# Kernel tuning notes

Hardware: AMD Instinct MI355X
Metric: run time of the kernel (lower is better)

## Reference

```python
import jax, jax.numpy as jnp
import numpy as np

IN_F = 4096
OUT_F = 4096
SPARSITY = 0.9
NNZ = round((1.0 - SPARSITY) * IN_F * OUT_F)  # 1677722
BATCH = 4096


def setup_inputs() -> dict:
    key = jax.random.key(0)
    k1, k2, k3, k4 = jax.random.split(key, 4)
    x = jax.random.normal(k1, (BATCH, IN_F), dtype=jnp.float32)
    # Kaiming-ish scale for sparse fan-in
    weights = jax.random.normal(k2, (NNZ,), dtype=jnp.float32) * 0.02
    row = jax.random.randint(k3, (NNZ,), 0, OUT_F, dtype=jnp.int32)
    col = jax.random.randint(k4, (NNZ,), 0, IN_F, dtype=jnp.int32)
    indices = jnp.stack([row, col], axis=0)  # (2, nnz) like the torch buffer
    active_mask = jnp.ones((NNZ,), dtype=bool)
    return {
        "x": x,
        "weights": weights,
        "indices": indices,
        "active_mask": active_mask,
        "out_features": OUT_F,
        "in_features": IN_F,
    }


def reference(x, weights, indices, active_mask, out_features, in_features):
    # Torch forward: select active edges, build COO (out,in), coalesce
    # (sums duplicate indices), then y = (W @ x^T)^T.
    # Equivalent math: zero inactive weights, scatter-add into dense W,
    # then a dense matmul. Duplicates are summed by .add, matching coalesce.
    w = jnp.where(active_mask, weights, jnp.zeros((), dtype=weights.dtype))
    W = jnp.zeros((out_features, in_features), dtype=x.dtype)
    W = W.at[indices[0], indices[1]].add(w)  # (out, in)
    return x @ W.T  # (B, out)
```

## Files before the change

### kernel.cpp

```cpp
#include <hip/hip_runtime.h>
#include <cstdint>
#include <cstddef>

#define IN_F  4096
#define OUT_F 4096
#define BATCH 4096

typedef __bf16 bf16_t;
typedef __bf16 bf16x8 __attribute__((ext_vector_type(8)));
typedef float  f32x4  __attribute__((ext_vector_type(4)));

__device__ __forceinline__ unsigned short f32_to_bf16_rne(float f) {
  union { float f; unsigned int u; } v;
  v.f = f;
  unsigned int u = v.u;
  return (unsigned short)((u + 0x7FFFu + ((u >> 16) & 1u)) >> 16);
}

__device__ __forceinline__ uint4 cvt8(float4 a, float4 b) {
  uint4 o;
  o.x = (unsigned)f32_to_bf16_rne(a.x) | ((unsigned)f32_to_bf16_rne(a.y) << 16);
  o.y = (unsigned)f32_to_bf16_rne(a.z) | ((unsigned)f32_to_bf16_rne(a.w) << 16);
  o.z = (unsigned)f32_to_bf16_rne(b.x) | ((unsigned)f32_to_bf16_rne(b.y) << 16);
  o.w = (unsigned)f32_to_bf16_rne(b.z) | ((unsigned)f32_to_bf16_rne(b.w) << 16);
  return o;
}

#define WU16 ((OUT_F * IN_F) / 8)
#define XUNITS ((BATCH * IN_F) / 8)

__global__ __launch_bounds__(256) void init_zero_cvtx(
    uint4* __restrict__ Wbfv, const float4* __restrict__ xin,
    uint4* __restrict__ xbf) {
  const uint4 z = {0u, 0u, 0u, 0u};
  for (int u = blockIdx.x * 256 + threadIdx.x; u < WU16 + XUNITS;
       u += gridDim.x * 256) {
    if (u < WU16) {
      Wbfv[u] = z;
    } else {
      const int i = u - WU16;
      xbf[i] = cvt8(xin[2 * i], xin[2 * i + 1]);
    }
  }
}

__global__ __launch_bounds__(256) void scatter_bf16(
    const float* __restrict__ w, const int* __restrict__ rows,
    const int* __restrict__ cols, const int* __restrict__ mask,
    unsigned* __restrict__ Wpk, int nnz) {
  int i = blockIdx.x * 256 + threadIdx.x;
  if (i >= nnz) return;
  if (mask[i] == 0) return;
  const unsigned h = f32_to_bf16_rne(w[i]);
  const size_t e = (size_t)rows[i] * IN_F + cols[i];
  const unsigned data = (e & 1) ? (h << 16) : h;
  unsigned* p = Wpk + (e >> 1);
  asm volatile("global_atomic_pk_add_bf16 %0, %1, off"
               :: "v"(p), "v"(data) : "memory");
}

#define A0_B 0
#define B0_B 32768
#define A1_B 65536
#define B1_B 98304
#define HALF 16384

#define STAGE(Xg, kpos, ldsbase) do {                                          \
  __builtin_amdgcn_global_load_lds(                                            \
    (const __attribute__((address_space(1))) void*)((Xg) + (size_t)srow * 4096 + (kpos) + schunk), \
    (__attribute__((address_space(3))) void*)(lds + (ldsbase) + tid * 16), 16, 0, 0); \
  __builtin_amdgcn_global_load_lds(                                            \
    (const __attribute__((address_space(1))) void*)((Xg) + (size_t)(srow + 128) * 4096 + (kpos) + schunk), \
    (__attribute__((address_space(3))) void*)(lds + (ldsbase) + 8192 + tid * 16), 16, 0, 0); \
} while (0)

#define LDALL(ab, bb) do {                                                     \
  a0 = *(const bf16x8*)(lds + (ab) + offA[0][0]);                              \
  a1 = *(const bf16x8*)(lds + (ab) + offA[0][1]);                              \
  a2 = *(const bf16x8*)(lds + (ab) + offA[0][2]);                              \
  a3 = *(const bf16x8*)(lds + (ab) + offA[0][3]);                              \
  a4 = *(const bf16x8*)(lds + (ab) + offA[1][0]);                              \
  a5 = *(const bf16x8*)(lds + (ab) + offA[1][1]);                              \
  a6 = *(const bf16x8*)(lds + (ab) + offA[1][2]);                              \
  a7 = *(const bf16x8*)(lds + (ab) + offA[1][3]);                              \
  b0 = *(const bf16x8*)(lds + (bb) + offB[0]);                                 \
  b1 = *(const bf16x8*)(lds + (bb) + offB[1]);                                 \
  b2 = *(const bf16x8*)(lds + (bb) + offB[2]);                                 \
  b3 = *(const bf16x8*)(lds + (bb) + offB[3]);                                 \
} while (0)

#define MQ(mh, A0_, A1_, A2_, A3_) do {                                        \
  acc[(mh)*4+0][0] = __builtin_amdgcn_mfma_f32_16x16x32_bf16(A0_, b0, acc[(mh)*4+0][0], 0, 0, 0); \
  acc[(mh)*4+0][1] = __builtin_amdgcn_mfma_f32_16x16x32_bf16(A0_, b1, acc[(mh)*4+0][1], 0, 0, 0); \
  acc[(mh)*4+0][2] = __builtin_amdgcn_mfma_f32_16x16x32_bf16(A0_, b2, acc[(mh)*4+0][2], 0, 0, 0); \
  acc[(mh)*4+0][3] = __builtin_amdgcn_mfma_f32_16x16x32_bf16(A0_, b3, acc[(mh)*4+0][3], 0, 0, 0); \
  acc[(mh)*4+1][0] = __builtin_amdgcn_mfma_f32_16x16x32_bf16(A1_, b0, acc[(mh)*4+1][0], 0, 0, 0); \
  acc[(mh)*4+1][1] = __builtin_amdgcn_mfma_f32_16x16x32_bf16(A1_, b1, acc[(mh)*4+1][1], 0, 0, 0); \
  acc[(mh)*4+1][2] = __builtin_amdgcn_mfma_f32_16x16x32_bf16(A1_, b2, acc[(mh)*4+1][2], 0, 0, 0); \
  acc[(mh)*4+1][3] = __builtin_amdgcn_mfma_f32_16x16x32_bf16(A1_, b3, acc[(mh)*4+1][3], 0, 0, 0); \
  acc[(mh)*4+2][0] = __builtin_amdgcn_mfma_f32_16x16x32_bf16(A2_, b0, acc[(mh)*4+2][0], 0, 0, 0); \
  acc[(mh)*4+2][1] = __builtin_amdgcn_mfma_f32_16x16x32_bf16(A2_, b1, acc[(mh)*4+2][1], 0, 0, 0); \
  acc[(mh)*4+2][2] = __builtin_amdgcn_mfma_f32_16x16x32_bf16(A2_, b2, acc[(mh)*4+2][2], 0, 0, 0); \
  acc[(mh)*4+2][3] = __builtin_amdgcn_mfma_f32_16x16x32_bf16(A2_, b3, acc[(mh)*4+2][3], 0, 0, 0); \
  acc[(mh)*4+3][0] = __builtin_amdgcn_mfma_f32_16x16x32_bf16(A3_, b0, acc[(mh)*4+3][0], 0, 0, 0); \
  acc[(mh)*4+3][1] = __builtin_amdgcn_mfma_f32_16x16x32_bf16(A3_, b1, acc[(mh)*4+3][1], 0, 0, 0); \
  acc[(mh)*4+3][2] = __builtin_amdgcn_mfma_f32_16x16x32_bf16(A3_, b2, acc[(mh)*4+3][2], 0, 0, 0); \
  acc[(mh)*4+3][3] = __builtin_amdgcn_mfma_f32_16x16x32_bf16(A3_, b3, acc[(mh)*4+3][3], 0, 0, 0); \
} while (0)

#define MFMA32() do { MQ(0, a0, a1, a2, a3); MQ(1, a4, a5, a6, a7); } while (0)

#define BAR()   __builtin_amdgcn_s_barrier()
#define LGKM0() do { asm volatile("s_waitcnt lgkmcnt(0)" ::: "memory");        \
                     __builtin_amdgcn_sched_barrier(0); } while (0)
#define VM(n)   asm volatile("s_waitcnt vmcnt(" #n ")" ::: "memory")
#define PRIO1() __builtin_amdgcn_s_setprio(1)
#define PRIO0() __builtin_amdgcn_s_setprio(0)

__global__ __launch_bounds__(512, 2) void gemm_bt_4ph(
    const bf16_t* __restrict__ A, const bf16_t* __restrict__ Bm,
    float* __restrict__ C) {
  __shared__ __align__(16) char lds[131072];

  const int tid  = threadIdx.x;
  const int lane = tid & 63;
  const int wave = tid >> 6;
  const int wm   = wave >> 2;
  const int wn   = wave & 3;

  const int sbid = (blockIdx.x & 7) * 32 + (blockIdx.x >> 3);
  const int bm   = sbid >> 4;
  const int bn   = sbid & 15;

  const int frow = lane & 15;
  const int c16  = (lane >> 4) * 16;

  int offA[2][4], offB[4];
#pragma unroll
  for (int mh = 0; mh < 2; ++mh)
#pragma unroll
    for (int mi = 0; mi < 4; ++mi) {
      int r = wm * 128 + mh * 64 + mi * 16 + frow;
      offA[mh][mi] = r * 64 + (c16 ^ (((r >> 1) & 3) << 4));
    }
#pragma unroll
  for (int ni = 0; ni < 4; ++ni) {
    int r = wn * 64 + ni * 16 + frow;
    offB[ni] = r * 64 + (c16 ^ (((r >> 1) & 3) << 4));
  }

  const int srow   = tid >> 2;
  const int schunk = ((tid & 3) ^ ((srow >> 1) & 3)) * 8;
  const bf16_t* Ag = A  + (size_t)bm * 256 * 4096;
  const bf16_t* Bg = Bm + (size_t)bn * 256 * 4096;

  f32x4 acc[8][4] = {};
  bf16x8 a0, a1, a2, a3, a4, a5, a6, a7, b0, b1, b2, b3;

  STAGE(Ag, 0,  A0_B);
  STAGE(Bg, 0,  B0_B);
  STAGE(Ag, 32, A0_B + HALF);
  STAGE(Bg, 32, B0_B + HALF);
  STAGE(Ag, 64, A1_B);
  STAGE(Bg, 64, B1_B);
  VM(8);
  BAR();

  int kb = 0;
#pragma unroll 1
  for (int i = 0; i < 31; ++i, kb += 128) {
    LDALL(A0_B, B0_B);
    STAGE(Ag, kb + 96, A1_B + HALF);
    STAGE(Bg, kb + 96, B1_B + HALF);
    BAR(); LGKM0(); PRIO1(); MFMA32(); PRIO0(); VM(8); BAR();
    LDALL(A0_B + HALF, B0_B + HALF);
    STAGE(Ag, kb + 128, A0_B);
    STAGE(Bg, kb + 128, B0_B);
    BAR(); LGKM0(); PRIO1(); MFMA32(); PRIO0(); VM(8); BAR();
    LDALL(A1_B, B1_B);
    STAGE(Ag, kb + 160, A0_B + HALF);
    STAGE(Bg, kb + 160, B0_B + HALF);
    BAR(); LGKM0(); PRIO1(); MFMA32(); PRIO0(); VM(8); BAR();
    LDALL(A1_B + HALF, B1_B + HALF);
    STAGE(Ag, kb + 192, A1_B);
    STAGE(Bg, kb + 192, B1_B);
    BAR(); LGKM0(); PRIO1(); MFMA32(); PRIO0(); VM(8); BAR();
  }

  LDALL(A0_B, B0_B);
  STAGE(Ag, 4064, A1_B + HALF);
  STAGE(Bg, 4064, B1_B + HALF);
  BAR(); LGKM0(); PRIO1(); MFMA32(); PRIO0(); VM(8); BAR();
  LDALL(A0_B + HALF, B0_B + HALF);
  BAR(); LGKM0(); PRIO1(); MFMA32(); PRIO0(); VM(4); BAR();
  LDALL(A1_B, B1_B);
  BAR(); LGKM0(); PRIO1(); MFMA32(); PRIO0(); VM(0); BAR();
  LDALL(A1_B + HALF, B1_B + HALF);
  LGKM0(); PRIO1(); MFMA32(); PRIO0();

#pragma unroll
  for (int mh = 0; mh < 2; ++mh)
#pragma unroll
    for (int mi = 0; mi < 4; ++mi)
#pragma unroll
      for (int ni = 0; ni < 4; ++ni) {
        const int row = bm * 256 + wm * 128 + mh * 64 + mi * 16 + (lane >> 4) * 4;
        const int col = bn * 256 + wn * 64 + ni * 16 + frow;
#pragma unroll
        for (int jj = 0; jj < 4; ++jj)
          C[(size_t)(row + jj) * 4096 + col] = acc[mh * 4 + mi][ni][jj];
      }
}

extern "C" void kernel_launch(void* const* d_in, const int* in_sizes, int n_in,
                              void* d_out, int out_size, void* d_ws, size_t ws_size,
                              hipStream_t stream) {
  const float* x     = (const float*)d_in[0];
  const float* wvals = (const float*)d_in[1];
  const int*   idx   = (const int*)d_in[2];
  const int*   mk    = (const int*)d_in[3];
  const int    nnz   = in_sizes[1];

  bf16_t* Wbf = (bf16_t*)d_ws;
  bf16_t* xbf = (bf16_t*)((char*)d_ws + (size_t)OUT_F * IN_F * sizeof(bf16_t));

  const size_t needed = (size_t)OUT_F * IN_F * 2 + (size_t)BATCH * IN_F * 2;
  if (ws_size < needed) return;

  init_zero_cvtx<<<2048, 256, 0, stream>>>(
      (uint4*)Wbf, (const float4*)x, (uint4*)xbf);

  scatter_bf16<<<(nnz + 255) / 256, 256, 0, stream>>>(
      wvals, idx, idx + nnz, mk, (unsigned*)Wbf, nnz);

  gemm_bt_4ph<<<256, 512, 0, stream>>>(xbf, Wbf, (float*)d_out);
}
```

Before: 212.3 us.

## Double-buffer LDS fragment registers to overlap LDS reads with MFMA

Splits the A/B fragment registers into two sets so that LDS reads for the next k-slice are issued while MFMAs consume the previous slice. Waits are relaxed to lgkmcnt(12) and vmcnt(4) so compute only waits for the older set. This removes the LDS-read latency exposed before each MFMA block, at the cost of 24 more VGPRs of fragments. With launch bounds of 2 waves per SIMD this may cause register pressure or spills, and it shifts the hazards between barriers and buffer reuse.

```diff
diff --git a/kernel.cpp b/kernel.cpp
--- a/kernel.cpp
+++ b/kernel.cpp
@@ -74,50 +74,53 @@
     (__attribute__((address_space(3))) void*)(lds + (ldsbase) + 8192 + tid * 16), 16, 0, 0); \
 } while (0)
 
-#define LDALL(ab, bb) do {                                                     \
-  a0 = *(const bf16x8*)(lds + (ab) + offA[0][0]);                              \
-  a1 = *(const bf16x8*)(lds + (ab) + offA[0][1]);                              \
-  a2 = *(const bf16x8*)(lds + (ab) + offA[0][2]);                              \
-  a3 = *(const bf16x8*)(lds + (ab) + offA[0][3]);                              \
-  a4 = *(const bf16x8*)(lds + (ab) + offA[1][0]);                              \
-  a5 = *(const bf16x8*)(lds + (ab) + offA[1][1]);                              \
-  a6 = *(const bf16x8*)(lds + (ab) + offA[1][2]);                              \
-  a7 = *(const bf16x8*)(lds + (ab) + offA[1][3]);                              \
-  b0 = *(const bf16x8*)(lds + (bb) + offB[0]);                                 \
-  b1 = *(const bf16x8*)(lds + (bb) + offB[1]);                                 \
-  b2 = *(const bf16x8*)(lds + (bb) + offB[2]);                                 \
-  b3 = *(const bf16x8*)(lds + (bb) + offB[3]);                                 \
-} while (0)
-
-#define MQ(mh, A0_, A1_, A2_, A3_) do {                                        \
-  acc[(mh)*4+0][0] = __builtin_amdgcn_mfma_f32_16x16x32_bf16(A0_, b0, acc[(mh)*4+0][0], 0, 0, 0); \
-  acc[(mh)*4+0][1] = __builtin_amdgcn_mfma_f32_16x16x32_bf16(A0_, b1, acc[(mh)*4+0][1], 0, 0, 0); \
-  acc[(mh)*4+0][2] = __builtin_amdgcn_mfma_f32_16x16x32_bf16(A0_, b2, acc[(mh)*4+0][2], 0, 0, 0); \
-  acc[(mh)*4+0][3] = __builtin_amdgcn_mfma_f32_16x16x32_bf16(A0_, b3, acc[(mh)*4+0][3], 0, 0, 0); \
-  acc[(mh)*4+1][0] = __builtin_amdgcn_mfma_f32_16x16x32_bf16(A1_, b0, acc[(mh)*4+1][0], 0, 0, 0); \
-  acc[(mh)*4+1][1] = __builtin_amdgcn_mfma_f32_16x16x32_bf16(A1_, b1, acc[(mh)*4+1][1], 0, 0, 0); \
-  acc[(mh)*4+1][2] = __builtin_amdgcn_mfma_f32_16x16x32_bf16(A1_, b2, acc[(mh)*4+1][2], 0, 0, 0); \
-  acc[(mh)*4+1][3] = __builtin_amdgcn_mfma_f32_16x16x32_bf16(A1_, b3, acc[(mh)*4+1][3], 0, 0, 0); \
-  acc[(mh)*4+2][0] = __builtin_amdgcn_mfma_f32_16x16x32_bf16(A2_, b0, acc[(mh)*4+2][0], 0, 0, 0); \
-  acc[(mh)*4+2][1] = __builtin_amdgcn_mfma_f32_16x16x32_bf16(A2_, b1, acc[(mh)*4+2][1], 0, 0, 0); \
-  acc[(mh)*4+2][2] = __builtin_amdgcn_mfma_f32_16x16x32_bf16(A2_, b2, acc[(mh)*4+2][2], 0, 0, 0); \
-  acc[(mh)*4+2][3] = __builtin_amdgcn_mfma_f32_16x16x32_bf16(A2_, b3, acc[(mh)*4+2][3], 0, 0, 0); \
-  acc[(mh)*4+3][0] = __builtin_amdgcn_mfma_f32_16x16x32_bf16(A3_, b0, acc[(mh)*4+3][0], 0, 0, 0); \
-  acc[(mh)*4+3][1] = __builtin_amdgcn_mfma_f32_16x16x32_bf16(A3_, b1, acc[(mh)*4+3][1], 0, 0, 0); \
-  acc[(mh)*4+3][2] = __builtin_amdgcn_mfma_f32_16x16x32_bf16(A3_, b2, acc[(mh)*4+3][2], 0, 0, 0); \
-  acc[(mh)*4+3][3] = __builtin_amdgcn_mfma_f32_16x16x32_bf16(A3_, b3, acc[(mh)*4+3][3], 0, 0, 0); \
-} while (0)
-
-#define MFMA32() do { MQ(0, a0, a1, a2, a3); MQ(1, a4, a5, a6, a7); } while (0)
-
-#define BAR()   __builtin_amdgcn_s_barrier()
-#define LGKM0() do { asm volatile("s_waitcnt lgkmcnt(0)" ::: "memory");        \
-                     __builtin_amdgcn_sched_barrier(0); } while (0)
-#define VM(n)   asm volatile("s_waitcnt vmcnt(" #n ")" ::: "memory")
-#define PRIO1() __builtin_amdgcn_s_setprio(1)
-#define PRIO0() __builtin_amdgcn_s_setprio(0)
-
-__global__ __launch_bounds__(512, 2) void gemm_bt_4ph(
+#define RDSET(ab, bb, S) do {                                                  \
+  a##S##0 = *(const bf16x8*)(lds + (ab) + offA[0][0]);                         \
+  a##S##1 = *(const bf16x8*)(lds + (ab) + offA[0][1]);                         \
+  a##S##2 = *(const bf16x8*)(lds + (ab) + offA[0][2]);                         \
+  a##S##3 = *(const bf16x8*)(lds + (ab) + offA[0][3]);                         \
+  a##S##4 = *(const bf16x8*)(lds + (ab) + offA[1][0]);                         \
+  a##S##5 = *(const bf16x8*)(lds + (ab) + offA[1][1]);                         \
+  a##S##6 = *(const bf16x8*)(lds + (ab) + offA[1][2]);                         \
+  a##S##7 = *(const bf16x8*)(lds + (ab) + offA[1][3]);                         \
+  b##S##0 = *(const bf16x8*)(lds + (bb) + offB[0]);                            \
+  b##S##1 = *(const bf16x8*)(lds + (bb) + offB[1]);                            \
+  b##S##2 = *(const bf16x8*)(lds + (bb) + offB[2]);                            \
+  b##S##3 = *(const bf16x8*)(lds + (bb) + offB[3]);                            \
+} while (0)
+
+#define MQ(mh, A0_,A1_,A2_,A3_, B0_,B1_,B2_,B3_) do {                          \
+  acc[(mh)*4+0][0] = __builtin_amdgcn_mfma_f32_16x16x32_bf16(A0_, B0_, acc[(mh)*4+0][0], 0, 0, 0); \
+  acc[(mh)*4+0][1] = __builtin_amdgcn_mfma_f32_16x16x32_bf16(A0_, B1_, acc[(mh)*4+0][1], 0, 0, 0); \
+  acc[(mh)*4+0][2] = __builtin_amdgcn_mfma_f32_16x16x32_bf16(A0_, B2_, acc[(mh)*4+0][2], 0, 0, 0); \
+  acc[(mh)*4+0][3] = __builtin_amdgcn_mfma_f32_16x16x32_bf16(A0_, B3_, acc[(mh)*4+0][3], 0, 0, 0); \
+  acc[(mh)*4+1][0] = __builtin_amdgcn_mfma_f32_16x16x32_bf16(A1_, B0_, acc[(mh)*4+1][0], 0, 0, 0); \
+  acc[(mh)*4+1][1] = __builtin_amdgcn_mfma_f32_16x16x32_bf16(A1_, B1_, acc[(mh)*4+1][1], 0, 0, 0); \
+  acc[(mh)*4+1][2] = __builtin_amdgcn_mfma_f32_16x16x32_bf16(A1_, B2_, acc[(mh)*4+1][2], 0, 0, 0); \
+  acc[(mh)*4+1][3] = __builtin_amdgcn_mfma_f32_16x16x32_bf16(A1_, B3_, acc[(mh)*4+1][3], 0, 0, 0); \
+  acc[(mh)*4+2][0] = __builtin_amdgcn_mfma_f32_16x16x32_bf16(A2_, B0_, acc[(mh)*4+2][0], 0, 0, 0); \
+  acc[(mh)*4+2][1] = __builtin_amdgcn_mfma_f32_16x16x32_bf16(A2_, B1_, acc[(mh)*4+2][1], 0, 0, 0); \
+  acc[(mh)*4+2][2] = __builtin_amdgcn_mfma_f32_16x16x32_bf16(A2_, B2_, acc[(mh)*4+2][2], 0, 0, 0); \
+  acc[(mh)*4+2][3] = __builtin_amdgcn_mfma_f32_16x16x32_bf16(A2_, B3_, acc[(mh)*4+2][3], 0, 0, 0); \
+  acc[(mh)*4+3][0] = __builtin_amdgcn_mfma_f32_16x16x32_bf16(A3_, B0_, acc[(mh)*4+3][0], 0, 0, 0); \
+  acc[(mh)*4+3][1] = __builtin_amdgcn_mfma_f32_16x16x32_bf16(A3_, B1_, acc[(mh)*4+3][1], 0, 0, 0); \
+  acc[(mh)*4+3][2] = __builtin_amdgcn_mfma_f32_16x16x32_bf16(A3_, B2_, acc[(mh)*4+3][2], 0, 0, 0); \
+  acc[(mh)*4+3][3] = __builtin_amdgcn_mfma_f32_16x16x32_bf16(A3_, B3_, acc[(mh)*4+3][3], 0, 0, 0); \
+} while (0)
+
+#define MFMA32S(S) do {                                                        \
+  MQ(0, a##S##0,a##S##1,a##S##2,a##S##3, b##S##0,b##S##1,b##S##2,b##S##3);     \
+  MQ(1, a##S##4,a##S##5,a##S##6,a##S##7, b##S##0,b##S##1,b##S##2,b##S##3);     \
+} while (0)
+
+#define BAR()    __builtin_amdgcn_s_barrier()
+#define LGKMW(n) do { asm volatile("s_waitcnt lgkmcnt(" #n ")" ::: "memory");  \
+                      __builtin_amdgcn_sched_barrier(0); } while (0)
+#define VM(n)    asm volatile("s_waitcnt vmcnt(" #n ")" ::: "memory")
+#define PRIO1()  __builtin_amdgcn_s_setprio(1)
+#define PRIO0()  __builtin_amdgcn_s_setprio(0)
+
+__global__ __launch_bounds__(512, 2) void gemm_bt_ra(
     const bf16_t* __restrict__ A, const bf16_t* __restrict__ Bm,
     float* __restrict__ C) {
   __shared__ __align__(16) char lds[131072];
@@ -155,7 +158,8 @@
   const bf16_t* Bg = Bm + (size_t)bn * 256 * 4096;
 
   f32x4 acc[8][4] = {};
-  bf16x8 a0, a1, a2, a3, a4, a5, a6, a7, b0, b1, b2, b3;
+  bf16x8 aA0, aA1, aA2, aA3, aA4, aA5, aA6, aA7, bA0, bA1, bA2, bA3;
+  bf16x8 aB0, aB1, aB2, aB3, aB4, aB5, aB6, aB7, bB0, bB1, bB2, bB3;
 
   STAGE(Ag, 0,  A0_B);
   STAGE(Bg, 0,  B0_B);
@@ -163,40 +167,40 @@
   STAGE(Bg, 32, B0_B + HALF);
   STAGE(Ag, 64, A1_B);
   STAGE(Bg, 64, B1_B);
-  VM(8);
+  VM(4);
   BAR();
+  RDSET(A0_B, B0_B, A);
 
   int kb = 0;
 #pragma unroll 1
   for (int i = 0; i < 31; ++i, kb += 128) {
-    LDALL(A0_B, B0_B);
+    RDSET(A0_B + HALF, B0_B + HALF, B);
     STAGE(Ag, kb + 96, A1_B + HALF);
     STAGE(Bg, kb + 96, B1_B + HALF);
-    BAR(); LGKM0(); PRIO1(); MFMA32(); PRIO0(); VM(8); BAR();
-    LDALL(A0_B + HALF, B0_B + HALF);
+    BAR(); LGKMW(12); PRIO1(); MFMA32S(A); PRIO0(); VM(4); BAR();
+    RDSET(A1_B, B1_B, A);
     STAGE(Ag, kb + 128, A0_B);
     STAGE(Bg, kb + 128, B0_B);
-    BAR(); LGKM0(); PRIO1(); MFMA32(); PRIO0(); VM(8); BAR();
-    LDALL(A1_B, B1_B);
+    BAR(); LGKMW(12); PRIO1(); MFMA32S(B); PRIO0(); VM(4); BAR();
+    RDSET(A1_B + HALF, B1_B + HALF, B);
     STAGE(Ag, kb + 160, A0_B + HALF);
     STAGE(Bg, kb + 160, B0_B + HALF);
-    BAR(); LGKM0(); PRIO1(); MFMA32(); PRIO0(); VM(8); BAR();
-    LDALL(A1_B + HALF, B1_B + HALF);
+    BAR(); LGKMW(12); PRIO1(); MFMA32S(A); PRIO0(); VM(4); BAR();
+    RDSET(A0_B, B0_B, A);
     STAGE(Ag, kb + 192, A1_B);
     STAGE(Bg, kb + 192, B1_B);
-    BAR(); LGKM0(); PRIO1(); MFMA32(); PRIO0(); VM(8); BAR();
+    BAR(); LGKMW(12); PRIO1(); MFMA32S(B); PRIO0(); VM(4); BAR();
   }
 
-  LDALL(A0_B, B0_B);
+  RDSET(A0_B + HALF, B0_B + HALF, B);
   STAGE(Ag, 4064, A1_B + HALF);
   STAGE(Bg, 4064, B1_B + HALF);
-  BAR(); LGKM0(); PRIO1(); MFMA32(); PRIO0(); VM(8); BAR();
-  LDALL(A0_B + HALF, B0_B + HALF);
-  BAR(); LGKM0(); PRIO1(); MFMA32(); PRIO0(); VM(4); BAR();
-  LDALL(A1_B, B1_B);
-  BAR(); LGKM0(); PRIO1(); MFMA32(); PRIO0(); VM(0); BAR();
-  LDALL(A1_B + HALF, B1_B + HALF);
-  LGKM0(); PRIO1(); MFMA32(); PRIO0();
+  BAR(); LGKMW(12); PRIO1(); MFMA32S(A); PRIO0(); VM(4); BAR();
+  RDSET(A1_B, B1_B, A);
+  BAR(); LGKMW(12); PRIO1(); MFMA32S(B); PRIO0(); VM(0); BAR();
+  RDSET(A1_B + HALF, B1_B + HALF, B);
+  BAR(); LGKMW(12); PRIO1(); MFMA32S(A); PRIO0(); BAR();
+  LGKMW(0); PRIO1(); MFMA32S(B); PRIO0();
 
 #pragma unroll
   for (int mh = 0; mh < 2; ++mh)
@@ -233,5 +237,5 @@
   scatter_bf16<<<(nnz + 255) / 256, 256, 0, stream>>>(
       wvals, idx, idx + nnz, mk, (unsigned*)Wbf, nnz);
 
-  gemm_bt_4ph<<<256, 512, 0, stream>>>(xbf, Wbf, (float*)d_out);
-}
+  gemm_bt_ra<<<256, 512, 0, stream>>>(xbf, Wbf, (float*)d_out);
+}
```

Result: slower. 224.1 us (+5.6%).
